# Performance work log

Hardware: AMD Instinct MI355X
Metric: run time of the kernel (lower is better)

The kernel has to match this reference:

```python
import jax, jax.numpy as jnp
import numpy as np

HEADS = 8; DIM = 512; DHEAD = 64; INNER = HEADS * DHEAD
QB = 4; NTOK = 1024
GAMMA = 0.01; LAMBDA_REG = 0.001


def _ln(x, g, b, eps=1e-5):
    mu = x.mean(axis=-1, keepdims=True)
    var = x.var(axis=-1, keepdims=True)
    return (x - mu) / jnp.sqrt(var + eps) * g + b


def setup_inputs() -> dict:
    key = jax.random.key(0)
    ks = jax.random.split(key, 12)
    def w(k, shape, scale=0.02):
        return jax.random.normal(k, shape, dtype=jnp.float32) * scale
    return {
        'q': jax.random.normal(ks[0], (QB, NTOK, DIM), dtype=jnp.float32),
        'k': jax.random.normal(ks[1], (QB, NTOK, DIM), dtype=jnp.float32),
        'v': jax.random.normal(ks[2], (QB, NTOK, DIM), dtype=jnp.float32),
        'ln_in_g': jnp.ones((DIM,), jnp.float32),
        'ln_in_b': jnp.zeros((DIM,), jnp.float32),
        'W_in': w(ks[3], (DIM, INNER)),
        'wp_W1': w(ks[4], (2 * DHEAD, DHEAD)),
        'wp_b1': jnp.zeros((DHEAD,), jnp.float32),
        'wp_ln_g': jnp.ones((DHEAD,), jnp.float32),
        'wp_ln_b': jnp.zeros((DHEAD,), jnp.float32),
        'wp_W2': w(ks[5], (DHEAD, DHEAD // 2)),
        'wp_b2': jnp.zeros((DHEAD // 2,), jnp.float32),
        'wp_W3': w(ks[6], (DHEAD // 2, 3)),
        'wp_b3': jnp.zeros((3,), jnp.float32),
        'weight_temp': jnp.ones((1,), jnp.float32),
        'W_out': w(ks[7], (INNER, DIM)),
        'b_out': jnp.zeros((DIM,), jnp.float32),
    }


def _forward(q, k, v, ln_in_g, ln_in_b, W_in, wp_W1, wp_b1, wp_ln_g, wp_ln_b,
             wp_W2, wp_b2, wp_W3, wp_b3, weight_temp, W_out, b_out):
    def proj(t):  # [Q,N,DIM] -> [h,Q,N,d]
        y = _ln(t, ln_in_g, ln_in_b) @ W_in
        return y.reshape(t.shape[0], t.shape[1], HEADS, DHEAD).transpose(2, 0, 1, 3)
    f_q, f_k, f_v = proj(q), proj(k), proj(v)
    m = f_k.shape[2]
    sg = jax.lax.stop_gradient

    # --- cosine distance (clamped) ---
    dots = jnp.einsum('hqnd,hqmd->hqnm', f_q, f_k)
    n1 = jnp.linalg.norm(f_q, axis=-1, keepdims=True) + 1e-8   # [h,q,n,1]
    n2 = jnp.linalg.norm(f_k, axis=-1, keepdims=True) + 1e-8   # [h,q,m,1]
    cos = jnp.clip(dots / (n1 * jnp.swapaxes(n2, -1, -2)), -0.99, 0.99)

    # --- regularized covariance ---
    fkc = f_k - f_k.mean(axis=2, keepdims=True)
    fqc = f_q - f_q.mean(axis=-1, keepdims=True)
    cov = jnp.einsum('hqnd,hqmd->hqnm', fqc, fkc) / (DHEAD ** 0.5 + 1e-6)
    base_reg = LAMBDA_REG / max(m, 1)
    reg = jnp.where(jnp.std(cov, ddof=1) < 1e-6, base_reg * 10.0, base_reg)
    cov = jnp.clip(reg * cov, -50.0, 50.0)

    # --- margin-based variance (eval mode: adaptive_gamma = gamma) ---
    qn = f_q / jnp.maximum(jnp.linalg.norm(f_q, axis=-1, keepdims=True), 1e-6)
    kn = f_k / jnp.maximum(jnp.linalg.norm(f_k, axis=-1, keepdims=True), 1e-6)
    csim = jnp.clip(jnp.einsum('hqnd,hqmd->hqnm', qn, kn), -0.99, 0.99)
    margin = jnp.clip(GAMMA - csim, 0.0, 10.0)
    var_c = jnp.broadcast_to(margin.mean(axis=-1, keepdims=True), csim.shape)

    # --- dynamic per-head weight predictor (dropout off in eval) ---
    qg = f_q.mean(axis=(1, 2))          # [h,d]
    kg = f_k.mean(axis=(1, 2))
    feats = jnp.concatenate([qg, kg], axis=-1)          # [h,2d]
    h1 = jax.nn.relu(_ln(feats @ wp_W1 + wp_b1, wp_ln_g, wp_ln_b))
    h2 = jax.nn.relu(h1 @ wp_W2 + wp_b2)
    logits = jax.nn.softmax(h2 @ wp_W3 + wp_b3, axis=-1)  # Sequential ends with Softmax
    wt = jnp.clip(weight_temp, 0.1, 20.0)
    w = jax.nn.softmax(logits / wt, axis=-1)
    w = jnp.clip(w, 0.05, 0.8)
    w = w / w.sum(axis=-1, keepdims=True)                # [h,3]
    cw = w[:, 0].reshape(HEADS, 1, 1, 1)
    covw = w[:, 1].reshape(HEADS, 1, 1, 1)
    vw = w[:, 2].reshape(HEADS, 1, 1, 1)

    # --- normalize each component by its (detached) global std ---
    cn = sg(jnp.std(cos, ddof=1)) + 1e-6
    covn = sg(jnp.std(cov, ddof=1)) + 1e-6
    vn = sg(jnp.std(var_c, ddof=1)) + 1e-6
    cscale = jnp.where(cn < 1e-4, 0.1, 1.0)
    d2 = cw * (cos / cn * cscale) + covw * (cov / covn * 0.5) + vw * (var_c / vn * 0.5)
    dstd = jnp.std(d2, ddof=1)
    temp = jnp.where(dstd < 1e-6, 0.1, 0.3 + sg(dstd))
    d2 = d2 / jnp.clip(temp, 0.1, 5.0)

    attn = jax.nn.softmax(d2, axis=-1)
    out = jnp.einsum('hqnm,hqmd->hqnd', attn, f_v)
    out = out.transpose(1, 2, 0, 3).reshape(out.shape[1], out.shape[2], INNER)
    return out @ W_out + b_out


def reference(q, k, v, ln_in_g, ln_in_b, W_in, wp_W1, wp_b1, wp_ln_g, wp_ln_b,
              wp_W2, wp_b2, wp_W3, wp_b3, weight_temp, W_out, b_out):
    return _forward(q, k, v, ln_in_g, ln_in_b, W_in, wp_W1, wp_b1, wp_ln_g, wp_ln_b,
                    wp_W2, wp_b2, wp_W3, wp_b3, weight_temp, W_out, b_out)
```

## Files before the change

### kernel.cpp

```cpp
#include <hip/hip_runtime.h>
#include <math.h>

#define NH    8
#define NQB   4
#define NPAIR 32
#define NTOK  1024
#define DH    64
#define DIMX  512
#define NROWS (NPAIR*NTOK)

typedef __attribute__((ext_vector_type(8))) short short8;
typedef _Float16 half8 __attribute__((ext_vector_type(8)));
typedef __attribute__((ext_vector_type(4))) float f32x4;

__device__ __forceinline__ unsigned short f2bf(float x){
  unsigned u = __float_as_uint(x);
  u += 0x7fffu + ((u>>16)&1u);
  return (unsigned short)(u>>16);
}
__device__ __forceinline__ float bf2f(unsigned short h){
  return __uint_as_float(((unsigned)h)<<16);
}
__device__ __forceinline__ unsigned short f2h(float x){
  union{ _Float16 f; unsigned short u; } c; c.f = (_Float16)x; return c.u;
}
__device__ __forceinline__ float h2f(unsigned short u){
  union{ _Float16 f; unsigned short u; } c; c.u = u; return (float)c.f;
}
__device__ __forceinline__ f32x4 mfma16(short8 a, short8 b, f32x4 c){
  return __builtin_amdgcn_mfma_f32_16x16x32_bf16(a,b,c,0,0,0);
}
__device__ __forceinline__ f32x4 mfma16f(half8 a, half8 b, f32x4 c){
  return __builtin_amdgcn_mfma_f32_16x16x32_f16(a,b,c,0,0,0);
}
__device__ __forceinline__ void dma16(const void* g, void* l){
  __builtin_amdgcn_global_load_lds(
      (const __attribute__((address_space(1))) void*)g,
      (__attribute__((address_space(3))) void*)l, 16, 0, 0);
}

__device__ __forceinline__ size_t cidx(int r, int c){
  return ((((size_t)((r>>6)*8 + (c>>6)))*8 + ((c&63)>>3))*64 + (r&63))*8 + (c&7);
}
__device__ __forceinline__ size_t kidx(int p, int key, int dh){
  return ((((size_t)(p*16 + (key>>6)))*8 + (dh>>3))*64 + (key&63))*8 + (dh&7);
}


__global__ __launch_bounds__(256) void k_lnstats(const float* __restrict__ q,
    const float* __restrict__ k, const float* __restrict__ v,
    float* __restrict__ mu_rstd){
  int wid = threadIdx.x >> 6, lane = threadIdx.x & 63;
  int tok = blockIdx.x*4 + wid;
  const float* src = (tok < 4096) ? q : ((tok < 8192) ? k : v);
  int t = tok & 4095;
  const float4* p4 = (const float4*)(src + (size_t)t*DIMX) + lane*2;
  float4 a = p4[0], b = p4[1];
  float s  = a.x+a.y+a.z+a.w + b.x+b.y+b.z+b.w;
  float ss = a.x*a.x+a.y*a.y+a.z*a.z+a.w*a.w
           + b.x*b.x+b.y*b.y+b.z*b.z+b.w*b.w;
  #pragma unroll
  for (int off=32; off; off>>=1){ s += __shfl_down(s,off); ss += __shfl_down(ss,off); }
  if (lane==0){
    float mu = s*(1.0f/512.0f);
    float var = ss*(1.0f/512.0f) - mu*mu;
    mu_rstd[tok*2+0] = mu;
    mu_rstd[tok*2+1] = 1.0f/sqrtf(var + 1e-5f);
  }
}


__global__ __launch_bounds__(256) void k_splitW(const float* __restrict__ Wa,
    const float* __restrict__ Wb,
    unsigned short* __restrict__ Wth, unsigned short* __restrict__ Wtl,
    unsigned short* __restrict__ Woth, unsigned short* __restrict__ Wotl){
  __shared__ float tile[64][65];
  int z = blockIdx.z;
  const float* W = z ? Wb : Wa;
  unsigned short* oh_ = z ? Woth : Wth;
  unsigned short* ol_ = z ? Wotl : Wtl;
  int kb = blockIdx.x, nb = blockIdx.y, tid = threadIdx.x;
  #pragma unroll
  for (int it=0; it<4; ++it){
    int idx = tid + 256*it;
    int kr = idx>>4, c4 = idx&15;
    float4 vv = *(const float4*)(W + (size_t)(kb*64+kr)*DIMX + nb*64 + c4*4);
    tile[c4*4+0][kr]=vv.x; tile[c4*4+1][kr]=vv.y; tile[c4*4+2][kr]=vv.z; tile[c4*4+3][kr]=vv.w;
  }
  __syncthreads();
  #pragma unroll
  for (int it=0; it<4; ++it){
    int idx = tid + 256*it;
    int n = idx>>4, k4 = idx&15;
    size_t base = cidx(nb*64+n, kb*64+k4*4);
    ushort4 hv, lv;
    { float xx=tile[n][k4*4+0]; unsigned short hh=f2bf(xx); hv.x=hh; lv.x=f2bf(xx-bf2f(hh)); }
    { float xx=tile[n][k4*4+1]; unsigned short hh=f2bf(xx); hv.y=hh; lv.y=f2bf(xx-bf2f(hh)); }
    { float xx=tile[n][k4*4+2]; unsigned short hh=f2bf(xx); hv.z=hh; lv.z=f2bf(xx-bf2f(hh)); }
    { float xx=tile[n][k4*4+3]; unsigned short hh=f2bf(xx); hv.w=hh; lv.w=f2bf(xx-bf2f(hh)); }
    *(ushort4*)(oh_+base) = hv;
    *(ushort4*)(ol_+base) = lv;
  }
}


__global__ __launch_bounds__(256) void k_projmm(
    const float* __restrict__ q, const float* __restrict__ k, const float* __restrict__ v,
    const float* __restrict__ g, const float* __restrict__ bln,
    const unsigned short* __restrict__ Wth, const unsigned short* __restrict__ Wtl,
    const float* __restrict__ mu_rstd,
    unsigned short* __restrict__ fqh, unsigned short* __restrict__ fql,
    unsigned short* __restrict__ fkh, unsigned short* __restrict__ fkl,
    float* __restrict__ fv,
    double* __restrict__ qgs, double* __restrict__ nusum){
  __shared__ __align__(16) unsigned short Ahs[64*72];
  __shared__ __align__(16) unsigned short Als[64*72];
  __shared__ __align__(16) unsigned short WhL[2][4096];
  __shared__ __align__(16) unsigned short WlL[2][4096];
  __shared__ float scrc[4][128];
  int z = blockIdx.z;
  const float* x = (z==0) ? q : ((z==1) ? k : v);
  int mb = blockIdx.x, nb = blockIdx.y;
  int tid = threadIdx.x, w = tid>>6, l = tid&63, lm = l&15, qd = l>>4;
  int rbase = (w&1)*32;
  int tile = w>>1;
  int cbase = nb*128 + tile*64;
  scrc[tid>>7][tid&127] = 0.f;
  scrc[2+(tid>>7)][tid&127] = 0.f;
  f32x4 acc[2][4];
  #pragma unroll
  for (int mt=0;mt<2;++mt)
    #pragma unroll
    for (int nt=0;nt<4;++nt) acc[mt][nt] = (f32x4){0.f,0.f,0.f,0.f};
  for (int kc8 = 0; kc8 < 8; ++kc8){
    float4 xv[4]; float mus[4], rss[4]; float4 gv[4], bv[4]; int rr[4], kk4[4];
    #pragma unroll
    for (int it=0; it<4; ++it){
      int idx = tid + 256*it;
      int r = idx>>4, k4 = idx&15;
      rr[it]=r; kk4[it]=k4;
      int tokg = z*4096 + mb*64 + r;
      mus[it] = mu_rstd[tokg*2+0]; rss[it] = mu_rstd[tokg*2+1];
      xv[it] = *(const float4*)(x + (size_t)(mb*64+r)*DIMX + kc8*64 + k4*4);
      gv[it] = *(const float4*)(g   + kc8*64 + k4*4);
      bv[it] = *(const float4*)(bln + kc8*64 + k4*4);
    }
    __syncthreads();
    {
      int st = w>>1, hl = w&1;
      const unsigned short* src = (hl ? Wtl : Wth)
          + ((size_t)((nb*2+st)*8 + kc8))*4096;
      unsigned short* dst = hl ? WlL[st] : WhL[st];
      #pragma unroll
      for (int j=0;j<8;++j) dma16(src + j*512 + l*8, dst + j*512);
    }
    #pragma unroll
    for (int it=0; it<4; ++it){
      float y0 = (xv[it].x-mus[it])*rss[it]*gv[it].x + bv[it].x;
      float y1 = (xv[it].y-mus[it])*rss[it]*gv[it].y + bv[it].y;
      float y2 = (xv[it].z-mus[it])*rss[it]*gv[it].z + bv[it].z;
      float y3 = (xv[it].w-mus[it])*rss[it]*gv[it].w + bv[it].w;
      ushort4 hv, lv;
      { unsigned short hh=f2bf(y0); hv.x=hh; lv.x=f2bf(y0-bf2f(hh)); }
      { unsigned short hh=f2bf(y1); hv.y=hh; lv.y=f2bf(y1-bf2f(hh)); }
      { unsigned short hh=f2bf(y2); hv.z=hh; lv.z=f2bf(y2-bf2f(hh)); }
      { unsigned short hh=f2bf(y3); hv.w=hh; lv.w=f2bf(y3-bf2f(hh)); }
      *(ushort4*)(Ahs + rr[it]*72 + kk4[it]*4) = hv;
      *(ushort4*)(Als + rr[it]*72 + kk4[it]*4) = lv;
    }
    __syncthreads();
    #pragma unroll
    for (int kch=0; kch<2; ++kch){
      short8 a_h[2], a_l[2];
      #pragma unroll
      for (int mt=0;mt<2;++mt){
        a_h[mt] = *(const short8*)(Ahs + (rbase+mt*16+lm)*72 + kch*32 + qd*8);
        a_l[mt] = *(const short8*)(Als + (rbase+mt*16+lm)*72 + kch*32 + qd*8);
      }
      #pragma unroll
      for (int nt=0;nt<4;++nt){
        int off = ((kch*4+qd)*64 + nt*16+lm)*8;
        short8 bh = *(const short8*)(WhL[tile] + off);
        short8 bl = *(const short8*)(WlL[tile] + off);
        #pragma unroll
        for (int mt=0;mt<2;++mt){
          acc[mt][nt] = mfma16(a_h[mt], bh, acc[mt][nt]);
          acc[mt][nt] = mfma16(a_h[mt], bl, acc[mt][nt]);
          acc[mt][nt] = mfma16(a_l[mt], bh, acc[mt][nt]);
        }
      }
    }
  }
  int head = cbase >> 6;
  if (z < 2){
    float csum[4] = {0.f,0.f,0.f,0.f};
    #pragma unroll
    for (int mt=0;mt<2;++mt){
      #pragma unroll
      for (int nt=0;nt<4;++nt){
        #pragma unroll
        for (int i=0;i<4;++i){
          float val = acc[mt][nt][i];
          csum[nt] += val;
          int tglob = mb*64 + rbase + mt*16 + qd*4 + i;
          int qb = tglob>>10, n = tglob&1023;
          int p = head*4 + qb;
          int d = nt*16 + lm;
          unsigned short hh = f2bf(val);
          unsigned short ll = f2bf(val - bf2f(hh));
          if (z==0){
            size_t ix = ((size_t)(p*NTOK+n))*DH + d;
            fqh[ix] = hh; fql[ix] = ll;
          } else {
            size_t ix = kidx(p, n, d);
            fkh[ix] = hh; fkl[ix] = ll;
          }
        }
      }
    }
    #pragma unroll
    for (int m=16;m<64;m<<=1){
      #pragma unroll
      for (int nt=0;nt<4;++nt) csum[nt] += __shfl_xor(csum[nt], m);
    }
    if (qd==0){
      #pragma unroll
      for (int nt=0;nt<4;++nt) scrc[w][tile*64 + nt*16 + lm] = csum[nt];
    }
    __syncthreads();
    if (tid < 128){
      float s = scrc[0][tid]+scrc[1][tid]+scrc[2][tid]+scrc[3][tid];
      if (z==0){
        atomicAdd(&qgs[nb*128 + tid], (double)s);
      } else {
        int col = nb*128 + tid;
        int hh2 = col>>6, d = col&63;
        int qb = mb>>4;
        atomicAdd(&nusum[(size_t)(hh2*4+qb)*DH + d], (double)s);
      }
    }
  } else {
    #pragma unroll
    for (int mt=0;mt<2;++mt){
      #pragma unroll
      for (int nt=0;nt<4;++nt){
        #pragma unroll
        for (int i=0;i<4;++i){
          int tglob = mb*64 + rbase + mt*16 + qd*4 + i;
          int qb = tglob>>10, n = tglob&1023;
          int p = head*4 + qb;
          int d = nt*16 + lm;
          fv[((size_t)(p*NTOK+n))*DH + d] = acc[mt][nt][i];
        }
      }
    }
  }
}


__global__ __launch_bounds__(256) void k_vT(const float* __restrict__ fv,
    unsigned short* __restrict__ fvTh, unsigned short* __restrict__ fvTl){
  __shared__ float tile[64][65];
  int mc = blockIdx.x, p = blockIdx.y, tid = threadIdx.x;
  #pragma unroll
  for (int it=0; it<4; ++it){
    int idx = tid + 256*it;
    int m = idx>>4, d4 = idx&15;
    float4 vv = *(const float4*)(fv + ((size_t)(p*NTOK + mc*64 + m)*DH + d4*4));
    tile[d4*4+0][m]=vv.x; tile[d4*4+1][m]=vv.y; tile[d4*4+2][m]=vv.z; tile[d4*4+3][m]=vv.w;
  }
  __syncthreads();
  #pragma unroll
  for (int it=0; it<2; ++it){
    int idx = tid + 256*it;
    int d = idx>>3, seg = idx&7;
    size_t base = ((((size_t)(p*16+mc))*8 + seg)*64 + d)*8;
    ushort4 h0,h1,l0,l1;
    { float xx=tile[d][seg*8+0]; unsigned short hh=f2h(xx); h0.x=hh; l0.x=f2h(xx-h2f(hh)); }
    { float xx=tile[d][seg*8+1]; unsigned short hh=f2h(xx); h0.y=hh; l0.y=f2h(xx-h2f(hh)); }
    { float xx=tile[d][seg*8+2]; unsigned short hh=f2h(xx); h0.z=hh; l0.z=f2h(xx-h2f(hh)); }
    { float xx=tile[d][seg*8+3]; unsigned short hh=f2h(xx); h0.w=hh; l0.w=f2h(xx-h2f(hh)); }
    { float xx=tile[d][seg*8+4]; unsigned short hh=f2h(xx); h1.x=hh; l1.x=f2h(xx-h2f(hh)); }
    { float xx=tile[d][seg*8+5]; unsigned short hh=f2h(xx); h1.y=hh; l1.y=f2h(xx-h2f(hh)); }
    { float xx=tile[d][seg*8+6]; unsigned short hh=f2h(xx); h1.z=hh; l1.z=f2h(xx-h2f(hh)); }
    { float xx=tile[d][seg*8+7]; unsigned short hh=f2h(xx); h1.w=hh; l1.w=f2h(xx-h2f(hh)); }
    *(ushort4*)(fvTh+base)   = h0;
    *(ushort4*)(fvTh+base+4) = h1;
    *(ushort4*)(fvTl+base)   = l0;
    *(ushort4*)(fvTl+base+4) = l1;
  }
}


__global__ __launch_bounds__(256) void k_rows(
    const unsigned short* __restrict__ fqh, const unsigned short* __restrict__ fql,
    const unsigned short* __restrict__ fkh, const unsigned short* __restrict__ fkl,
    const double* __restrict__ nusum,
    float* __restrict__ inv_na_q, float* __restrict__ muqA, float* __restrict__ tqA,
    float* __restrict__ inv_na_k, float* __restrict__ skA){
  int wid = threadIdx.x >> 6, lane = threadIdx.x & 63;
  int row = blockIdx.x*4 + wid;
  int p = row >> 10;
  int key = row & 1023;
  size_t ix = (size_t)row*DH + lane;
  float xq = bf2f(fqh[ix]) + bf2f(fql[ix]);
  float nv = (float)(nusum[(size_t)p*DH + lane] * (1.0/1024.0));
  float s = xq, ss = xq*xq, sd = xq*nv;
  #pragma unroll
  for (int off=32; off; off>>=1){
    s += __shfl_down(s,off); ss += __shfl_down(ss,off); sd += __shfl_down(sd,off);
  }
  if (lane==0){
    float nrm = sqrtf(ss);
    inv_na_q[row] = 1.0f/(nrm+1e-8f);
    muqA[row] = s*(1.0f/64.0f);
    tqA[row] = sd;
  }
  size_t ixk = kidx(p, key, lane);
  float xk = bf2f(fkh[ixk]) + bf2f(fkl[ixk]);
  float s2 = xk, ss2 = xk*xk;
  #pragma unroll
  for (int off=32; off; off>>=1){
    s2 += __shfl_down(s2,off); ss2 += __shfl_down(ss2,off);
  }
  if (lane==0){
    float nrm = sqrtf(ss2);
    inv_na_k[row] = 1.0f/(nrm+1e-8f);
    skA[row] = s2;
  }
}


__global__ __launch_bounds__(256) void k_wp(const double* __restrict__ qgs,
    const double* __restrict__ nusum,
    const float* __restrict__ W1, const float* __restrict__ b1,
    const float* __restrict__ lgv, const float* __restrict__ lbv,
    const float* __restrict__ W2, const float* __restrict__ b2,
    const float* __restrict__ W3, const float* __restrict__ b3,
    const float* __restrict__ wtemp, float* __restrict__ wp_out,
    float* __restrict__ Sarr){
  __shared__ float feats[8][128];
  __shared__ float h1[8][64];
  __shared__ float h2s[8][32];
  __shared__ float lgt[8][3];
  __shared__ float mv[8][2];
  int tid = threadIdx.x;
  for (int idx = tid; idx < 1024; idx += 256){
    int h = idx >> 7, i = idx & 127;
    double vv;
    if (i < 64){
      vv = qgs[h*64+i];
    } else {
      int d = i - 64;
      vv = nusum[(size_t)(h*4+0)*DH+d] + nusum[(size_t)(h*4+1)*DH+d]
         + nusum[(size_t)(h*4+2)*DH+d] + nusum[(size_t)(h*4+3)*DH+d];
    }
    feats[h][i] = (float)(vv * (1.0/4096.0));
  }
  if (tid < 32){
    double s = 0.0;
    for (int d = 0; d < 64; ++d) s += nusum[(size_t)tid*DH + d];
    Sarr[tid] = (float)(s * (1.0/1024.0));
  }
  __syncthreads();
  for (int idx = tid; idx < 512; idx += 256){
    int h = idx >> 6, j = idx & 63;
    float s = b1[j];
    for (int i = 0; i < 128; ++i) s += feats[h][i]*W1[i*64+j];
    h1[h][j] = s;
  }
  __syncthreads();
  if (tid < 8){
    float s=0.f, ss=0.f;
    for (int j=0;j<64;++j){ float vv=h1[tid][j]; s+=vv; ss+=vv*vv; }
    float mu = s*(1.0f/64.0f);
    float var = ss*(1.0f/64.0f)-mu*mu;
    mv[tid][0]=mu; mv[tid][1]=1.0f/sqrtf(var+1e-5f);
  }
  __syncthreads();
  for (int idx = tid; idx < 512; idx += 256){
    int h = idx>>6, j = idx&63;
    float vv = (h1[h][j]-mv[h][0])*mv[h][1]*lgv[j] + lbv[j];
    h1[h][j] = fmaxf(vv, 0.f);
  }
  __syncthreads();
  {
    int h = tid >> 5, j = tid & 31;
    float s = b2[j];
    for (int i=0;i<64;++i) s += h1[h][i]*W2[i*32+j];
    h2s[h][j] = fmaxf(s, 0.f);
  }
  __syncthreads();
  if (tid < 24){
    int h = tid/3, j = tid - h*3;
    float s = b3[j];
    for (int i=0;i<32;++i) s += h2s[h][i]*W3[i*3+j];
    lgt[h][j] = s;
  }
  __syncthreads();
  if (tid < 8){
    int h = tid;
    float z0=lgt[h][0], z1=lgt[h][1], z2=lgt[h][2];
    float m = fmaxf(z0,fmaxf(z1,z2));
    float e0=expf(z0-m), e1=expf(z1-m), e2=expf(z2-m);
    float inv = 1.0f/(e0+e1+e2);
    float l0=e0*inv, l1=e1*inv, l2=e2*inv;
    float wt = fminf(fmaxf(wtemp[0], 0.1f), 20.0f);
    float y0=l0/wt, y1=l1/wt, y2=l2/wt;
    float m2 = fmaxf(y0,fmaxf(y1,y2));
    float f0=expf(y0-m2), f1=expf(y1-m2), f2=expf(y2-m2);
    float inv2 = 1.0f/(f0+f1+f2);
    float w0=f0*inv2, w1=f1*inv2, w2=f2*inv2;
    w0 = fminf(fmaxf(w0,0.05f),0.8f);
    w1 = fminf(fmaxf(w1,0.05f),0.8f);
    w2 = fminf(fmaxf(w2,0.05f),0.8f);
    float isum = 1.0f/(w0+w1+w2);
    wp_out[h*3+0]=w0*isum; wp_out[h*3+1]=w1*isum; wp_out[h*3+2]=w2*isum;
  }
}


__global__ __launch_bounds__(256) void k_passA(
    const unsigned short* __restrict__ fqh, const unsigned short* __restrict__ fql,
    const unsigned short* __restrict__ fkh, const unsigned short* __restrict__ fkl,
    const float* __restrict__ inv_na_q, const float* __restrict__ muqA,
    const float* __restrict__ tqA,
    const float* __restrict__ inv_na_k, const float* __restrict__ skA,
    const float* __restrict__ Sarr,
    float* __restrict__ rs_cos, float* __restrict__ rs_cov, float* __restrict__ rs_marg,
    float* __restrict__ mxcosA, float* __restrict__ mncosA,
    float* __restrict__ mxcovA, float* __restrict__ mncovA,
    double* __restrict__ gacc){
  __shared__ __align__(16) unsigned short Kh[4096];
  __shared__ __align__(16) unsigned short Kl[4096];
  __shared__ float redbuf[4][16][7];
  __shared__ double wredS[4][3];
  int b = blockIdx.x;
  int p = ((b&7)<<2) | ((b>>3)&3);
  int s = b>>5;
  int n0 = s*32;
  int tid = threadIdx.x, w = tid>>6, l = tid&63;
  int lm = l&15, q = l>>4;
  int rt = w&1, cw = w>>1;
  int nw = n0 + rt*16;
  float Sp = Sarr[p];
  const float inv8 = (float)(1.0/(8.0+1e-6));
  float ia[4], m8[4], t8[4];
  #pragma unroll
  for (int i=0;i<4;++i){
    int rg = p*NTOK + nw + q*4 + i;
    float mq = muqA[rg];
    ia[i] = inv_na_q[rg];
    m8[i] = mq*inv8;
    t8[i] = (tqA[rg] - mq*Sp)*inv8;
  }
  const short8* aqh = (const short8*)(fqh + (size_t)(p*NTOK + nw + lm)*DH);
  const short8* aql = (const short8*)(fql + (size_t)(p*NTOK + nw + lm)*DH);
  short8 ah0 = aqh[q], ah1 = aqh[4+q], al0 = aql[q], al1 = aql[4+q];
  const unsigned short* gKh = fkh + (size_t)p*16*4096;
  const unsigned short* gKl = fkl + (size_t)p*16*4096;
  const float* cAg = inv_na_k + p*NTOK;
  const float* cSg = skA + p*NTOK;
  float sc2=0.f, sv2=0.f, scv=0.f;
  float pc[4]={0,0,0,0}, pv_[4]={0,0,0,0}, pm[4]={0,0,0,0};
  float xc[4], nc[4], xv[4], nv[4];
  #pragma unroll
  for (int i=0;i<4;++i){ xc[i]=-1e30f; nc[i]=1e30f; xv[i]=-1e30f; nv[i]=1e30f; }
  for (int cc=0; cc<16; ++cc){
    __syncthreads();
    {
      int r = w*2;
      const unsigned short* cb = gKh + cc*4096;
      dma16(cb + (r  )*512 + l*8, &Kh[(r  )*512]);
      dma16(cb + (r+1)*512 + l*8, &Kh[(r+1)*512]);
      cb = gKl + cc*4096;
      dma16(cb + (r  )*512 + l*8, &Kl[(r  )*512]);
      dma16(cb + (r+1)*512 + l*8, &Kl[(r+1)*512]);
    }
    __syncthreads();
    #pragma unroll
    for (int t2=0; t2<2; ++t2){
      int c16 = cw*2 + t2;
      short8 kh0 = *(const short8*)&Kh[((q  )*64 + c16*16+lm)*8];
      short8 kh1 = *(const short8*)&Kh[((q+4)*64 + c16*16+lm)*8];
      short8 kl0 = *(const short8*)&Kl[((q  )*64 + c16*16+lm)*8];
      short8 kl1 = *(const short8*)&Kl[((q+4)*64 + c16*16+lm)*8];
      f32x4 acc = {0.f,0.f,0.f,0.f};
      acc = mfma16(ah0,kh0,acc); acc = mfma16(ah1,kh1,acc);
      acc = mfma16(al0,kh0,acc); acc = mfma16(al1,kh1,acc);
      acc = mfma16(ah0,kl0,acc); acc = mfma16(ah1,kl1,acc);
      int colg = cc*64 + c16*16 + lm;
      float ca = cAg[colg], cs = cSg[colg];
      #pragma unroll
      for (int i=0;i<4;++i){
        float dot = acc[i];
        float cosv = fminf(fmaxf(dot*ia[i]*ca,-0.99f),0.99f);
        float cov  = fmaf(-m8[i], cs, fmaf(dot, inv8, -t8[i]));
        float marg = fmaxf(0.01f - cosv, 0.f);
        sc2 = fmaf(cosv,cosv,sc2); sv2 = fmaf(cov,cov,sv2); scv = fmaf(cosv,cov,scv);
        pc[i]+=cosv; pv_[i]+=cov; pm[i]+=marg;
        xc[i]=fmaxf(xc[i],cosv); nc[i]=fminf(nc[i],cosv);
        xv[i]=fmaxf(xv[i],cov);  nv[i]=fminf(nv[i],cov);
      }
    }
  }
  #pragma unroll
  for (int m=1;m<16;m<<=1){
    #pragma unroll
    for (int i=0;i<4;++i){
      pc[i]+=__shfl_xor(pc[i],m); pv_[i]+=__shfl_xor(pv_[i],m); pm[i]+=__shfl_xor(pm[i],m);
      xc[i]=fmaxf(xc[i],__shfl_xor(xc[i],m)); nc[i]=fminf(nc[i],__shfl_xor(nc[i],m));
      xv[i]=fmaxf(xv[i],__shfl_xor(xv[i],m)); nv[i]=fminf(nv[i],__shfl_xor(nv[i],m));
    }
  }
  if (lm==0){
    #pragma unroll
    for (int i=0;i<4;++i){
      int r16 = q*4+i;
      redbuf[w][r16][0]=pc[i]; redbuf[w][r16][1]=pv_[i]; redbuf[w][r16][2]=pm[i];
      redbuf[w][r16][3]=xc[i]; redbuf[w][r16][4]=nc[i];
      redbuf[w][r16][5]=xv[i]; redbuf[w][r16][6]=nv[i];
    }
  }
  double vals[3] = {(double)sc2,(double)sv2,(double)scv};
  #pragma unroll
  for (int c2=0;c2<3;++c2){
    double vv = vals[c2];
    #pragma unroll
    for (int off=32; off; off>>=1) vv += __shfl_down(vv, off);
    if (l==0) wredS[w][c2] = vv;
  }
  __syncthreads();
  if (tid < 32){
    int rt2 = tid>>4, r16 = tid&15;
    int w0 = rt2, w1 = rt2+2;
    float sc = redbuf[w0][r16][0]+redbuf[w1][r16][0];
    float sv = redbuf[w0][r16][1]+redbuf[w1][r16][1];
    float sm = redbuf[w0][r16][2]+redbuf[w1][r16][2];
    float mxc = fmaxf(redbuf[w0][r16][3],redbuf[w1][r16][3]);
    float mnc = fminf(redbuf[w0][r16][4],redbuf[w1][r16][4]);
    float mxv = fmaxf(redbuf[w0][r16][5],redbuf[w1][r16][5]);
    float mnv = fminf(redbuf[w0][r16][6],redbuf[w1][r16][6]);
    int row = p*NTOK + n0 + tid;
    rs_cos[row]=sc; rs_cov[row]=sv; rs_marg[row]=sm;
    mxcosA[row]=mxc; mncosA[row]=mnc; mxcovA[row]=mxv; mncovA[row]=mnv;
  }
  if (tid == 0){
    int h = p >> 2;
    #pragma unroll
    for (int c2=0;c2<3;++c2){
      double t = wredS[0][c2]+wredS[1][c2]+wredS[2][c2]+wredS[3][c2];
      atomicAdd(&gacc[h*3+c2], t);
    }
  }
}


__global__ __launch_bounds__(256) void k_rowfin(const float* __restrict__ rs_cos,
    const float* __restrict__ rs_cov, const float* __restrict__ rs_marg,
    float* __restrict__ var_row, double* __restrict__ racc){
  __shared__ double wredS[4][6];
  int row = blockIdx.x*256 + threadIdx.x;
  int p = row >> 10; int h = p >> 2;
  float vr = rs_marg[row] * (1.0f/1024.0f);
  var_row[row] = vr;
  double dv = (double)vr;
  double rc = (double)rs_cos[row], rv = (double)rs_cov[row];
  double vals[6];
  vals[0] = 1024.0*dv;
  vals[1] = 1024.0*dv*dv;
  vals[2] = dv*rc;
  vals[3] = dv*rv;
  vals[4] = rc;
  vals[5] = rv;
  int lane = threadIdx.x & 63, wid = threadIdx.x >> 6;
  #pragma unroll
  for (int c2 = 0; c2 < 6; ++c2){
    double vv = vals[c2];
    #pragma unroll
    for (int off=32; off; off>>=1) vv += __shfl_down(vv, off);
    if (lane==0) wredS[wid][c2] = vv;
  }
  __syncthreads();
  if (threadIdx.x == 0){
    #pragma unroll
    for (int c2 = 0; c2 < 6; ++c2){
      double t = wredS[0][c2]+wredS[1][c2]+wredS[2][c2]+wredS[3][c2];
      atomicAdd(&racc[h*6+c2], t);
    }
  }
}


__global__ void k_final(const double* __restrict__ gacc, const double* __restrict__ racc,
                        const float* __restrict__ wp_out, float* __restrict__ coef){
  if (threadIdx.x != 0) return;
  const double N = 33554432.0;
  double Sc1=0,Sc2=0,Sv1=0,Sv2=0,Sr1=0,Sr2=0;
  for (int h=0;h<8;++h){
    Sc2+=gacc[h*3+0]; Sv2+=gacc[h*3+1];
    Sr1+=racc[h*6+0]; Sr2+=racc[h*6+1];
    Sc1+=racc[h*6+4]; Sv1+=racc[h*6+5];
  }
  double cvar = (Sc2 - Sc1*Sc1/N)/(N-1.0);
  double cn = sqrt(fmax(cvar,0.0)) + 1e-6;
  double cscale = (cn < 1e-4) ? 0.1 : 1.0;
  double vraw = (Sv2 - Sv1*Sv1/N)/(N-1.0);
  double sraw = sqrt(fmax(vraw,0.0));
  double basev = 0.001/1024.0;
  double regv = (sraw < 1e-6) ? basev*10.0 : basev;
  double covn = regv*sraw + 1e-6;
  double vvar = (Sr2 - Sr1*Sr1/N)/(N-1.0);
  double vn = sqrt(fmax(vvar,0.0)) + 1e-6;
  double ah[8], bh[8], chh[8];
  double Sd1=0.0, Sd2=0.0;
  for (int h=0;h<8;++h){
    double a = (double)wp_out[h*3+0]/cn*cscale;
    double b = (double)wp_out[h*3+1]*regv*0.5/covn;
    double c = (double)wp_out[h*3+2]*0.5/vn;
    ah[h]=a; bh[h]=b; chh[h]=c;
    Sd1 += a*racc[h*6+4] + b*racc[h*6+5] + c*racc[h*6+0];
    Sd2 += a*a*gacc[h*3+0] + b*b*gacc[h*3+1] + c*c*racc[h*6+1]
         + 2.0*(a*b*gacc[h*3+2] + a*c*racc[h*6+2] + b*c*racc[h*6+3]);
  }
  double dvar = (Sd2 - Sd1*Sd1/N)/(N-1.0);
  double dstd = sqrt(fmax(dvar,0.0));
  double temp = (dstd < 1e-6) ? 0.1 : 0.3 + dstd;
  double tcl = fmin(fmax(temp,0.1),5.0);
  double it = 1.0/tcl;
  for (int h=0;h<8;++h){
    coef[h*3+0] = (float)(ah[h]*it);
    coef[h*3+1] = (float)(bh[h]*it);
    coef[h*3+2] = (float)(chh[h]*it);
  }
}


__global__ __launch_bounds__(256) void k_pv(
    const unsigned short* __restrict__ fqh, const unsigned short* __restrict__ fql,
    const unsigned short* __restrict__ fkh, const unsigned short* __restrict__ fkl,
    const unsigned short* __restrict__ fvTh, const unsigned short* __restrict__ fvTl,
    const float* __restrict__ inv_na_q, const float* __restrict__ muqA,
    const float* __restrict__ tqA,
    const float* __restrict__ inv_na_k, const float* __restrict__ skA,
    const float* __restrict__ Sarr, const float* __restrict__ var_row,
    const float* __restrict__ mxcosA, const float* __restrict__ mncosA,
    const float* __restrict__ mxcovA, const float* __restrict__ mncovA,
    const float* __restrict__ coef,
    unsigned short* __restrict__ ohh, unsigned short* __restrict__ ohl){
  __shared__ __align__(16) unsigned short Kh[4096];
  __shared__ __align__(16) unsigned short Kl[4096];
  __shared__ __align__(16) unsigned short Vh[4096];
  __shared__ __align__(16) unsigned short Vl[4096];
  __shared__ __align__(16) unsigned short ph[32][72];
  __shared__ float denbuf[4][16];
  __shared__ float dnv[32];
  int b = blockIdx.x;
  int p = ((b&7)<<2) | ((b>>3)&3);
  int s = b>>5;
  int n0 = s*32;
  int h = p>>2, qb = p&3;
  int tid = threadIdx.x, w = tid>>6, l = tid&63;
  int lm = l&15, q = l>>4;
  int rt = w&1, cw = w>>1;
  int nw = n0 + rt*16;
  float A = coef[h*3+0], B = coef[h*3+1], C = coef[h*3+2];
  float Sp = Sarr[p];
  const float inv8 = (float)(1.0/(8.0+1e-6));
  float B8 = B*inv8;
  float ia[4], bm[4], o2[4];
  #pragma unroll
  for (int i=0;i<4;++i){
    int rg = p*NTOK + nw + q*4 + i;
    float mq = muqA[rg];
    ia[i] = inv_na_q[rg];
    bm[i] = B8*mq;
    float tq2 = tqA[rg] - mq*Sp;
    float vr = var_row[rg];
    float Mh = fmaxf(A*mxcosA[rg],A*mncosA[rg]) + fmaxf(B*mxcovA[rg],B*mncovA[rg]) + C*vr;
    o2[i] = (C*vr - Mh) - B8*tq2;
  }
  const short8* aqh = (const short8*)(fqh + (size_t)(p*NTOK + nw + lm)*DH);
  const short8* aql = (const short8*)(fql + (size_t)(p*NTOK + nw + lm)*DH);
  short8 ah0 = aqh[q], ah1 = aqh[4+q], al0 = aql[q], al1 = aql[4+q];
  const unsigned short* gKh = fkh  + (size_t)p*16*4096;
  const unsigned short* gKl = fkl  + (size_t)p*16*4096;
  const unsigned short* gVh = fvTh + (size_t)p*16*4096;
  const unsigned short* gVl = fvTl + (size_t)p*16*4096;
  const float* cAg = inv_na_k + p*NTOK;
  const float* cSg = skA + p*NTOK;
  f32x4 o0 = {0.f,0.f,0.f,0.f}, o1 = {0.f,0.f,0.f,0.f};
  float den[4] = {0.f,0.f,0.f,0.f};
  for (int cc = 0; cc < 16; ++cc){
    __syncthreads();
    {
      int r = w*2;
      const unsigned short* cb = gKh + cc*4096;
      dma16(cb + (r  )*512 + l*8, &Kh[(r  )*512]);
      dma16(cb + (r+1)*512 + l*8, &Kh[(r+1)*512]);
      cb = gKl + cc*4096;
      dma16(cb + (r  )*512 + l*8, &Kl[(r  )*512]);
      dma16(cb + (r+1)*512 + l*8, &Kl[(r+1)*512]);
      cb = gVh + cc*4096;
      dma16(cb + (r  )*512 + l*8, &Vh[(r  )*512]);
      dma16(cb + (r+1)*512 + l*8, &Vh[(r+1)*512]);
      cb = gVl + cc*4096;
      dma16(cb + (r  )*512 + l*8, &Vl[(r  )*512]);
      dma16(cb + (r+1)*512 + l*8, &Vl[(r+1)*512]);
    }
    __syncthreads();
    #pragma unroll
    for (int t2=0; t2<2; ++t2){
      int c16 = cw*2 + t2;
      short8 kh0 = *(const short8*)&Kh[((q  )*64 + c16*16+lm)*8];
      short8 kh1 = *(const short8*)&Kh[((q+4)*64 + c16*16+lm)*8];
      short8 kl0 = *(const short8*)&Kl[((q  )*64 + c16*16+lm)*8];
      short8 kl1 = *(const short8*)&Kl[((q+4)*64 + c16*16+lm)*8];
      f32x4 acc = {0.f,0.f,0.f,0.f};
      acc = mfma16(ah0,kh0,acc); acc = mfma16(ah1,kh1,acc);
      acc = mfma16(al0,kh0,acc); acc = mfma16(al1,kh1,acc);
      acc = mfma16(ah0,kl0,acc); acc = mfma16(ah1,kl1,acc);
      int colg = cc*64 + c16*16 + lm;
      float ca = cAg[colg], cs = cSg[colg];
      #pragma unroll
      for (int i=0;i<4;++i){
        float dot = acc[i];
        float cosv = fminf(fmaxf(dot*ia[i]*ca,-0.99f),0.99f);
        float arg = fmaf(A, cosv, fmaf(-bm[i], cs, fmaf(B8, dot, o2[i])));
        float e = __expf(arg);
        unsigned short us = f2h(e);
        ph[rt*16+q*4+i][c16*16+lm] = us;
        den[i] += h2f(us);
      }
    }
    __syncthreads();
    {
      half8 vh0 = *(const half8*)&Vh[((q  )*64 + w*16+lm)*8];
      half8 vh1 = *(const half8*)&Vh[((q+4)*64 + w*16+lm)*8];
      half8 vl0 = *(const half8*)&Vl[((q  )*64 + w*16+lm)*8];
      half8 vl1 = *(const half8*)&Vl[((q+4)*64 + w*16+lm)*8];
      half8 pb00 = *(const half8*)&ph[lm][q*8];
      half8 pb01 = *(const half8*)&ph[lm][32+q*8];
      half8 pb10 = *(const half8*)&ph[16+lm][q*8];
      half8 pb11 = *(const half8*)&ph[16+lm][32+q*8];
      o0 = mfma16f(vh0,pb00,o0); o0 = mfma16f(vl0,pb00,o0);
      o0 = mfma16f(vh1,pb01,o0); o0 = mfma16f(vl1,pb01,o0);
      o1 = mfma16f(vh0,pb10,o1); o1 = mfma16f(vl0,pb10,o1);
      o1 = mfma16f(vh1,pb11,o1); o1 = mfma16f(vl1,pb11,o1);
    }
  }
  #pragma unroll
  for (int m=1;m<16;m<<=1){
    #pragma unroll
    for (int i=0;i<4;++i) den[i] += __shfl_xor(den[i],m);
  }
  if (lm==0){
    #pragma unroll
    for (int i=0;i<4;++i) denbuf[w][q*4+i] = den[i];
  }
  __syncthreads();
  if (tid < 32){
    int rt2 = tid>>4, r16 = tid&15;
    dnv[tid] = 1.0f/(denbuf[rt2][r16] + denbuf[rt2+2][r16]);
  }
  __syncthreads();
  {
    float inv0 = dnv[lm];
    float inv1 = dnv[16+lm];
    int dcol = h*64 + w*16 + q*4;
    int row0 = qb*NTOK + n0 + lm;
    int row1 = row0 + 16;
    size_t b0i = cidx(row0, dcol);
    size_t b1i = cidx(row1, dcol);
    ushort4 h0,l0,h1,l1;
    { float xx=o0[0]*inv0; unsigned short hh=f2bf(xx); h0.x=hh; l0.x=f2bf(xx-bf2f(hh)); }
    { float xx=o0[1]*inv0; unsigned short hh=f2bf(xx); h0.y=hh; l0.y=f2bf(xx-bf2f(hh)); }
    { float xx=o0[2]*inv0; unsigned short hh=f2bf(xx); h0.z=hh; l0.z=f2bf(xx-bf2f(hh)); }
    { float xx=o0[3]*inv0; unsigned short hh=f2bf(xx); h0.w=hh; l0.w=f2bf(xx-bf2f(hh)); }
    { float xx=o1[0]*inv1; unsigned short hh=f2bf(xx); h1.x=hh; l1.x=f2bf(xx-bf2f(hh)); }
    { float xx=o1[1]*inv1; unsigned short hh=f2bf(xx); h1.y=hh; l1.y=f2bf(xx-bf2f(hh)); }
    { float xx=o1[2]*inv1; unsigned short hh=f2bf(xx); h1.z=hh; l1.z=f2bf(xx-bf2f(hh)); }
    { float xx=o1[3]*inv1; unsigned short hh=f2bf(xx); h1.w=hh; l1.w=f2bf(xx-bf2f(hh)); }
    *(ushort4*)(ohh+b0i)=h0; *(ushort4*)(ohl+b0i)=l0;
    *(ushort4*)(ohh+b1i)=h1; *(ushort4*)(ohl+b1i)=l1;
  }
}


__global__ __launch_bounds__(256) void k_outmm(
    const unsigned short* __restrict__ ohh, const unsigned short* __restrict__ ohl,
    const unsigned short* __restrict__ Woth, const unsigned short* __restrict__ Wotl,
    const float* __restrict__ bias, float* __restrict__ out){
  __shared__ __align__(16) unsigned short Ah[4096];
  __shared__ __align__(16) unsigned short Al[4096];
  __shared__ __align__(16) unsigned short W0h[4096];
  __shared__ __align__(16) unsigned short W0l[4096];
  __shared__ __align__(16) unsigned short W1h[4096];
  __shared__ __align__(16) unsigned short W1l[4096];
  int mb = blockIdx.x, nb = blockIdx.y;
  int tid = threadIdx.x, w = tid>>6, l = tid&63, lm = l&15, qd = l>>4;
  int rh = w&1, tile = w>>1;
  int cbase = nb*128 + tile*64;
  f32x4 acc[2][4];
  #pragma unroll
  for (int mt=0;mt<2;++mt)
    #pragma unroll
    for (int nt=0;nt<4;++nt) acc[mt][nt] = (f32x4){0.f,0.f,0.f,0.f};
  for (int kc8=0; kc8<8; ++kc8){
    __syncthreads();
    {
      const unsigned short* aSh = ohh  + ((size_t)(mb*8+kc8))*4096;
      const unsigned short* aSl = ohl  + ((size_t)(mb*8+kc8))*4096;
      const unsigned short* s0h = Woth + ((size_t)((nb*2  )*8+kc8))*4096;
      const unsigned short* s0l = Wotl + ((size_t)((nb*2  )*8+kc8))*4096;
      const unsigned short* s1h = Woth + ((size_t)((nb*2+1)*8+kc8))*4096;
      const unsigned short* s1l = Wotl + ((size_t)((nb*2+1)*8+kc8))*4096;
      if (w==0){
        #pragma unroll
        for (int j=0;j<8;++j) dma16(aSh + j*512 + l*8, &Ah[j*512]);
        #pragma unroll
        for (int j=0;j<4;++j) dma16(s1h + j*512 + l*8, &W1h[j*512]);
      } else if (w==1){
        #pragma unroll
        for (int j=0;j<8;++j) dma16(aSl + j*512 + l*8, &Al[j*512]);
        #pragma unroll
        for (int j=4;j<8;++j) dma16(s1h + j*512 + l*8, &W1h[j*512]);
      } else if (w==2){
        #pragma unroll
        for (int j=0;j<8;++j) dma16(s0h + j*512 + l*8, &W0h[j*512]);
        #pragma unroll
        for (int j=0;j<4;++j) dma16(s1l + j*512 + l*8, &W1l[j*512]);
      } else {
        #pragma unroll
        for (int j=0;j<8;++j) dma16(s0l + j*512 + l*8, &W0l[j*512]);
        #pragma unroll
        for (int j=4;j<8;++j) dma16(s1l + j*512 + l*8, &W1l[j*512]);
      }
    }
    __syncthreads();
    const unsigned short* Wh_ = tile ? W1h : W0h;
    const unsigned short* Wl_ = tile ? W1l : W0l;
    #pragma unroll
    for (int kch=0; kch<2; ++kch){
      short8 a_h[2], a_l[2];
      #pragma unroll
      for (int mt=0;mt<2;++mt){
        int off = ((kch*4+qd)*64 + rh*32 + mt*16 + lm)*8;
        a_h[mt] = *(const short8*)(Ah + off);
        a_l[mt] = *(const short8*)(Al + off);
      }
      #pragma unroll
      for (int nt=0;nt<4;++nt){
        int off = ((kch*4+qd)*64 + nt*16+lm)*8;
        short8 bh = *(const short8*)(Wh_ + off);
        short8 bl = *(const short8*)(Wl_ + off);
        #pragma unroll
        for (int mt=0;mt<2;++mt){
          acc[mt][nt] = mfma16(a_h[mt], bh, acc[mt][nt]);
          acc[mt][nt] = mfma16(a_h[mt], bl, acc[mt][nt]);
          acc[mt][nt] = mfma16(a_l[mt], bh, acc[mt][nt]);
        }
      }
    }
  }
  float bv[4];
  #pragma unroll
  for (int nt=0;nt<4;++nt) bv[nt] = bias[cbase+nt*16+lm];
  #pragma unroll
  for (int mt=0;mt<2;++mt){
    #pragma unroll
    for (int i=0;i<4;++i){
      int row = mb*64 + rh*32 + mt*16 + qd*4 + i;
      #pragma unroll
      for (int nt=0;nt<4;++nt){
        out[(size_t)row*DIMX + cbase + nt*16 + lm] = acc[mt][nt][i] + bv[nt];
      }
    }
  }
}


extern "C" void kernel_launch(void* const* d_in, const int* in_sizes, int n_in,
                              void* d_out, int out_size, void* d_ws, size_t ws_size,
                              hipStream_t stream) {
  (void)in_sizes; (void)n_in; (void)out_size;
  const float* q     = (const float*)d_in[0];
  const float* k     = (const float*)d_in[1];
  const float* v     = (const float*)d_in[2];
  const float* ln_g  = (const float*)d_in[3];
  const float* ln_b  = (const float*)d_in[4];
  const float* W_in  = (const float*)d_in[5];
  const float* wp_W1 = (const float*)d_in[6];
  const float* wp_b1 = (const float*)d_in[7];
  const float* wp_lg = (const float*)d_in[8];
  const float* wp_lb = (const float*)d_in[9];
  const float* wp_W2 = (const float*)d_in[10];
  const float* wp_b2 = (const float*)d_in[11];
  const float* wp_W3 = (const float*)d_in[12];
  const float* wp_b3 = (const float*)d_in[13];
  const float* wtemp = (const float*)d_in[14];
  const float* W_out = (const float*)d_in[15];
  const float* b_out = (const float*)d_in[16];
  float* out = (float*)d_out;

  char* wsb = (char*)d_ws;
  double* gacc = (double*)wsb;
  double* racc = gacc + 24;
  double* qgs  = racc + 48;
  double* nusum= qgs + 512;
  float* fvA = (float*)(wsb + 24576);
  unsigned short* ohh = (unsigned short*)fvA;
  unsigned short* ohl = ohh + (size_t)NQB*NTOK*NH*DH;
  float* mu_rstd = fvA + (size_t)NPAIR*NTOK*DH;
  float* Sarr = mu_rstd + 24576;
  float* inv_na_q = Sarr + 64;
  float* muqA     = inv_na_q + NROWS;
  float* tqA      = muqA + NROWS;
  float* inv_na_k = tqA + NROWS;
  float* skA      = inv_na_k + NROWS;
  float* rs_cos   = skA + NROWS;
  float* rs_cov   = rs_cos + NROWS;
  float* rs_marg  = rs_cov + NROWS;
  float* var_row  = rs_marg + NROWS;
  float* mxcos    = var_row + NROWS;
  float* mncos    = mxcos + NROWS;
  float* mxcov    = mncos + NROWS;
  float* mncov    = mxcov + NROWS;
  float* wp_out   = mncov + NROWS;
  float* coef     = wp_out + 32;
  float* endf     = coef + 32;
  size_t off16 = (size_t)((char*)endf - wsb);
  off16 = (off16 + 63) & ~(size_t)63;
  unsigned short* fqh  = (unsigned short*)(wsb + off16);
  unsigned short* fql  = fqh  + (size_t)NPAIR*NTOK*DH;
  unsigned short* fkh  = fql  + (size_t)NPAIR*NTOK*DH;
  unsigned short* fkl  = fkh  + (size_t)NPAIR*NTOK*DH;
  unsigned short* fvTh = fkl  + (size_t)NPAIR*NTOK*DH;
  unsigned short* fvTl = fvTh + (size_t)NPAIR*NTOK*DH;
  unsigned short* Wth  = fvTl + (size_t)NPAIR*NTOK*DH;
  unsigned short* Wtl  = Wth  + (size_t)DIMX*DIMX;
  unsigned short* Woth = Wtl  + (size_t)DIMX*DIMX;
  unsigned short* Wotl = Woth + (size_t)DIMX*DIMX;
  size_t need = (size_t)((char*)(Wotl + (size_t)DIMX*DIMX) - wsb);
  if (ws_size < need) return;

  hipMemsetAsync(wsb, 0, 24576, stream);
  k_lnstats<<<3072, 256, 0, stream>>>(q, k, v, mu_rstd);
  k_splitW<<<dim3(8,8,2), 256, 0, stream>>>(W_in, W_out, Wth, Wtl, Woth, Wotl);
  k_projmm<<<dim3(64,4,3), 256, 0, stream>>>(q, k, v, ln_g, ln_b, Wth, Wtl,
                                             mu_rstd, fqh, fql, fkh, fkl, fvA,
                                             qgs, nusum);
  k_vT<<<dim3(16,32), 256, 0, stream>>>(fvA, fvTh, fvTl);
  k_rows<<<8192, 256, 0, stream>>>(fqh, fql, fkh, fkl, nusum,
                                   inv_na_q, muqA, tqA, inv_na_k, skA);
  k_wp<<<1, 256, 0, stream>>>(qgs, nusum, wp_W1, wp_b1, wp_lg, wp_lb,
                              wp_W2, wp_b2, wp_W3, wp_b3, wtemp, wp_out, Sarr);
  k_passA<<<1024, 256, 0, stream>>>(fqh, fql, fkh, fkl,
                                    inv_na_q, muqA, tqA, inv_na_k, skA, Sarr,
                                    rs_cos, rs_cov, rs_marg,
                                    mxcos, mncos, mxcov, mncov, gacc);
  k_rowfin<<<128, 256, 0, stream>>>(rs_cos, rs_cov, rs_marg, var_row, racc);
  k_final<<<1, 64, 0, stream>>>(gacc, racc, wp_out, coef);
  k_pv<<<1024, 256, 0, stream>>>(fqh, fql, fkh, fkl, fvTh, fvTl,
                                 inv_na_q, muqA, tqA, inv_na_k, skA, Sarr,
                                 var_row, mxcos, mncos, mxcov, mncov, coef,
                                 ohh, ohl);
  k_outmm<<<dim3(64,4), 256, 0, stream>>>(ohh, ohl, Woth, Wotl, b_out, out);
}
```

Baseline: 276.9 us.

## Load K/V fragments directly from global memory and double-buffer P tile

In passA and the PV kernel, the per-chunk staging of K (and V) into shared memory via DMA, with its two barriers per iteration, is removed. Each lane now reads its MFMA fragments straight from global memory, relying on the pre-tiled layout and L2/L1 caching. The probability tile is double-buffered by chunk parity so one barrier per iteration is enough. This removes barrier overhead and LDS traffic and frees LDS for occupancy, at the cost of redundant global/cache reads across waves and exposed global load latency.

```diff
diff --git a/kernel.cpp b/kernel.cpp
--- a/kernel.cpp
+++ b/kernel.cpp
@@ -431,8 +431,6 @@
     float* __restrict__ mxcosA, float* __restrict__ mncosA,
     float* __restrict__ mxcovA, float* __restrict__ mncovA,
     double* __restrict__ gacc){
-  __shared__ __align__(16) unsigned short Kh[4096];
-  __shared__ __align__(16) unsigned short Kl[4096];
   __shared__ float redbuf[4][16][7];
   __shared__ double wredS[4][3];
   int b = blockIdx.x;
@@ -466,25 +464,18 @@
   float xc[4], nc[4], xv[4], nv[4];
   #pragma unroll
   for (int i=0;i<4;++i){ xc[i]=-1e30f; nc[i]=1e30f; xv[i]=-1e30f; nv[i]=1e30f; }
+  int ko0 = ((q  )*64 + (cw*2  )*16+lm)*8;
+  int ko1 = ((q+4)*64 + (cw*2  )*16+lm)*8;
   for (int cc=0; cc<16; ++cc){
-    __syncthreads();
-    {
-      int r = w*2;
-      const unsigned short* cb = gKh + cc*4096;
-      dma16(cb + (r  )*512 + l*8, &Kh[(r  )*512]);
-      dma16(cb + (r+1)*512 + l*8, &Kh[(r+1)*512]);
-      cb = gKl + cc*4096;
-      dma16(cb + (r  )*512 + l*8, &Kl[(r  )*512]);
-      dma16(cb + (r+1)*512 + l*8, &Kl[(r+1)*512]);
-    }
-    __syncthreads();
+    const unsigned short* cbh = gKh + cc*4096;
+    const unsigned short* cbl = gKl + cc*4096;
     #pragma unroll
     for (int t2=0; t2<2; ++t2){
       int c16 = cw*2 + t2;
-      short8 kh0 = *(const short8*)&Kh[((q  )*64 + c16*16+lm)*8];
-      short8 kh1 = *(const short8*)&Kh[((q+4)*64 + c16*16+lm)*8];
-      short8 kl0 = *(const short8*)&Kl[((q  )*64 + c16*16+lm)*8];
-      short8 kl1 = *(const short8*)&Kl[((q+4)*64 + c16*16+lm)*8];
+      short8 kh0 = *(const short8*)(cbh + ko0 + t2*128);
+      short8 kh1 = *(const short8*)(cbh + ko1 + t2*128);
+      short8 kl0 = *(const short8*)(cbl + ko0 + t2*128);
+      short8 kl1 = *(const short8*)(cbl + ko1 + t2*128);
       f32x4 acc = {0.f,0.f,0.f,0.f};
       acc = mfma16(ah0,kh0,acc); acc = mfma16(ah1,kh1,acc);
       acc = mfma16(al0,kh0,acc); acc = mfma16(al1,kh1,acc);
@@ -648,11 +639,7 @@
     const float* __restrict__ mxcovA, const float* __restrict__ mncovA,
     const float* __restrict__ coef,
     unsigned short* __restrict__ ohh, unsigned short* __restrict__ ohl){
-  __shared__ __align__(16) unsigned short Kh[4096];
-  __shared__ __align__(16) unsigned short Kl[4096];
-  __shared__ __align__(16) unsigned short Vh[4096];
-  __shared__ __align__(16) unsigned short Vl[4096];
-  __shared__ __align__(16) unsigned short ph[32][72];
+  __shared__ __align__(16) unsigned short ph[2][32][72];
   __shared__ float denbuf[4][16];
   __shared__ float dnv[32];
   int b = blockIdx.x;
@@ -691,31 +678,21 @@
   const float* cSg = skA + p*NTOK;
   f32x4 o0 = {0.f,0.f,0.f,0.f}, o1 = {0.f,0.f,0.f,0.f};
   float den[4] = {0.f,0.f,0.f,0.f};
+  int ko0 = ((q  )*64 + (cw*2)*16+lm)*8;
+  int ko1 = ((q+4)*64 + (cw*2)*16+lm)*8;
+  int vo0 = ((q  )*64 + w*16+lm)*8;
+  int vo1 = ((q+4)*64 + w*16+lm)*8;
   for (int cc = 0; cc < 16; ++cc){
-    __syncthreads();
-    {
-      int r = w*2;
-      const unsigned short* cb = gKh + cc*4096;
-      dma16(cb + (r  )*512 + l*8, &Kh[(r  )*512]);
-      dma16(cb + (r+1)*512 + l*8, &Kh[(r+1)*512]);
-      cb = gKl + cc*4096;
-      dma16(cb + (r  )*512 + l*8, &Kl[(r  )*512]);
-      dma16(cb + (r+1)*512 + l*8, &Kl[(r+1)*512]);
-      cb = gVh + cc*4096;
-      dma16(cb + (r  )*512 + l*8, &Vh[(r  )*512]);
-      dma16(cb + (r+1)*512 + l*8, &Vh[(r+1)*512]);
-      cb = gVl + cc*4096;
-      dma16(cb + (r  )*512 + l*8, &Vl[(r  )*512]);
-      dma16(cb + (r+1)*512 + l*8, &Vl[(r+1)*512]);
-    }
-    __syncthreads();
+    const unsigned short* cbh = gKh + cc*4096;
+    const unsigned short* cbl = gKl + cc*4096;
+    unsigned short (*phc)[72] = ph[cc&1];
     #pragma unroll
     for (int t2=0; t2<2; ++t2){
       int c16 = cw*2 + t2;
-      short8 kh0 = *(const short8*)&Kh[((q  )*64 + c16*16+lm)*8];
-      short8 kh1 = *(const short8*)&Kh[((q+4)*64 + c16*16+lm)*8];
-      short8 kl0 = *(const short8*)&Kl[((q  )*64 + c16*16+lm)*8];
-      short8 kl1 = *(const short8*)&Kl[((q+4)*64 + c16*16+lm)*8];
+      short8 kh0 = *(const short8*)(cbh + ko0 + t2*128);
+      short8 kh1 = *(const short8*)(cbh + ko1 + t2*128);
+      short8 kl0 = *(const short8*)(cbl + ko0 + t2*128);
+      short8 kl1 = *(const short8*)(cbl + ko1 + t2*128);
       f32x4 acc = {0.f,0.f,0.f,0.f};
       acc = mfma16(ah0,kh0,acc); acc = mfma16(ah1,kh1,acc);
       acc = mfma16(al0,kh0,acc); acc = mfma16(al1,kh1,acc);
@@ -729,20 +706,22 @@
         float arg = fmaf(A, cosv, fmaf(-bm[i], cs, fmaf(B8, dot, o2[i])));
         float e = __expf(arg);
         unsigned short us = f2h(e);
-        ph[rt*16+q*4+i][c16*16+lm] = us;
+        phc[rt*16+q*4+i][c16*16+lm] = us;
         den[i] += h2f(us);
       }
     }
+    const unsigned short* cvh = gVh + cc*4096;
+    const unsigned short* cvl = gVl + cc*4096;
+    half8 vh0 = *(const half8*)(cvh + vo0);
+    half8 vh1 = *(const half8*)(cvh + vo1);
+    half8 vl0 = *(const half8*)(cvl + vo0);
+    half8 vl1 = *(const half8*)(cvl + vo1);
     __syncthreads();
     {
-      half8 vh0 = *(const half8*)&Vh[((q  )*64 + w*16+lm)*8];
-      half8 vh1 = *(const half8*)&Vh[((q+4)*64 + w*16+lm)*8];
-      half8 vl0 = *(const half8*)&Vl[((q  )*64 + w*16+lm)*8];
-      half8 vl1 = *(const half8*)&Vl[((q+4)*64 + w*16+lm)*8];
-      half8 pb00 = *(const half8*)&ph[lm][q*8];
-      half8 pb01 = *(const half8*)&ph[lm][32+q*8];
-      half8 pb10 = *(const half8*)&ph[16+lm][q*8];
-      half8 pb11 = *(const half8*)&ph[16+lm][32+q*8];
+      half8 pb00 = *(const half8*)&phc[lm][q*8];
+      half8 pb01 = *(const half8*)&phc[lm][32+q*8];
+      half8 pb10 = *(const half8*)&phc[16+lm][q*8];
+      half8 pb11 = *(const half8*)&phc[16+lm][32+q*8];
       o0 = mfma16f(vh0,pb00,o0); o0 = mfma16f(vl0,pb00,o0);
       o0 = mfma16f(vh1,pb01,o0); o0 = mfma16f(vl1,pb01,o0);
       o1 = mfma16f(vh0,pb10,o1); o1 = mfma16f(vl0,pb10,o1);
```

Measured after the change: 263.1 us. 1.05x faster.
